# Kernel tuning notes

Measured on AMD Instinct MI355X. Metric: run time of the kernel, lower is better.

## Reference

```python
import jax, jax.numpy as jnp
import numpy as np

N = 100000      # nodes_num
E = 1600000     # edges (avg degree 16)
D_IN = 256
D_OUT = 128
EPS = 1e-3      # keras BatchNormalization default epsilon
LEAKY = 0.2     # tf.nn.leaky_relu default alpha


def setup_inputs() -> dict:
    key = jax.random.key(0)
    ks = jax.random.split(key, 6)
    x = jax.random.normal(ks[0], (N, D_IN), jnp.float32)
    w = jax.random.normal(ks[1], (D_IN, D_OUT), jnp.float32) / np.float32(np.sqrt(D_IN))
    w1 = jax.random.normal(ks[2], (D_IN, D_IN), jnp.float32) / np.float32(np.sqrt(D_IN))
    w2 = jax.random.normal(ks[3], (D_IN, D_IN), jnp.float32) / np.float32(np.sqrt(D_IN))
    rows = jnp.sort(jax.random.randint(ks[4], (E,), 0, N, jnp.int32))
    cols = jax.random.randint(ks[5], (E,), 0, N, jnp.int32)
    edge_vals = jnp.ones((E,), jnp.float32)
    return {"x": x, "w": w, "w1": w1, "w2": w2,
            "edge_vals": edge_vals, "rows": rows, "cols": cols}


def reference(x, w, w1, w2, edge_vals, rows, cols):
    # Batch norm (training mode: per-feature stats over node axis, gamma=1, beta=0)
    mean = jnp.mean(x, axis=0)
    var = jnp.var(x, axis=0)
    xn = (x - mean) * jax.lax.rsqrt(var + EPS)          # [N, D_IN]

    mapped = xn @ w                                      # [N, D_OUT]
    s1 = jnp.tanh(jnp.sum((xn @ w1) * xn, axis=1))       # [N] row score
    s2 = jnp.tanh(jnp.sum((xn @ w2) * xn, axis=1))       # [N] col score

    # sparse add of adj*s1[row] and adj*s2[col], then leaky_relu on edge values
    ev = edge_vals * (s1[rows] + s2[cols])               # [E]
    ev = jnp.where(ev > 0, ev, LEAKY * ev)

    # tf.sparse.softmax: softmax over the nonzero entries of each row
    m = jax.ops.segment_max(ev, rows, num_segments=N)    # [N]
    m = jnp.where(jnp.isfinite(m), m, 0.0)               # empty rows -> 0
    ex = jnp.exp(ev - m[rows])
    denom = jax.ops.segment_sum(ex, rows, num_segments=N)
    alpha = ex / denom[rows]                             # [E] edge softmax

    # SpMM: out[i] = sum_{e: rows[e]==i} alpha[e] * mapped[cols[e]]
    out = jax.ops.segment_sum(alpha[:, None] * mapped[cols], rows, num_segments=N)
    return out  # activation is identity (activation=None)
```

## Files before the change

### kernel.cpp

```cpp
#include <hip/hip_runtime.h>

#define D_IN 256
#define D_OUT 128
#define EPS_BN 1e-3f
#define LEAKY 0.2f

typedef unsigned short u16;
typedef unsigned int u32;
typedef u16 u16x4 __attribute__((ext_vector_type(4)));
typedef u16 u16x8 __attribute__((ext_vector_type(8)));
typedef __bf16 bf16x8 __attribute__((ext_vector_type(8)));
typedef float f32x4 __attribute__((ext_vector_type(4)));

__device__ __forceinline__ float bf2f(u16 u) {
    u32 v = ((u32)u) << 16;
    return __uint_as_float(v);
}
__device__ __forceinline__ u16 f2bf(float f) {
    u32 u = __float_as_uint(f);
    u32 r = (u + 0x7FFFu + ((u >> 16) & 1u)) >> 16;
    return (u16)r;
}

__device__ __forceinline__ void bar_lgkm() {
    asm volatile("s_waitcnt lgkmcnt(0)" ::: "memory");
    __builtin_amdgcn_s_barrier();
    asm volatile("" ::: "memory");
}

__global__ void colstats_k(const float* __restrict__ x, int n,
                           float* __restrict__ sums, float* __restrict__ sqs) {
    int c = threadIdx.x;
    float s = 0.f, q = 0.f;
    for (int r = blockIdx.x; r < n; r += gridDim.x) {
        float v = x[(size_t)r * D_IN + c];
        s += v;
        q += v * v;
    }
    atomicAdd(&sums[c], s);
    atomicAdd(&sqs[c], q);
}

__global__ void finalize_k(const float* __restrict__ sums, const float* __restrict__ sqs,
                           int n, float* __restrict__ mean, float* __restrict__ inv) {
    int c = threadIdx.x;
    float m = sums[c] / (float)n;
    float v = sqs[c] / (float)n - m * m;
    mean[c] = m;
    inv[c] = rsqrtf(v + EPS_BN);
}

__global__ void prep_w_k(const float* __restrict__ w1, const float* __restrict__ w2,
                         const float* __restrict__ w, u16* __restrict__ Bth,
                         u16* __restrict__ Btl, u16* __restrict__ Wth,
                         u16* __restrict__ Wtl) {
    int idx = blockIdx.x * 256 + threadIdx.x;
    int k = idx & 255;
    int nn = idx >> 8;
    if (nn < 512) {
        float v = (nn < 256) ? w1[(size_t)k * 256 + nn]
                             : w2[(size_t)k * 256 + (nn - 256)];
        u16 h = f2bf(v);
        u16 l = f2bf(v - bf2f(h));
        Bth[(size_t)nn * 256 + k] = h;
        Btl[(size_t)nn * 256 + k] = l;
    } else {
        int nm = nn - 512;
        float v = w[(size_t)k * D_OUT + nm];
        u16 h = f2bf(v);
        u16 l = f2bf(v - bf2f(h));
        Wth[(size_t)nm * 256 + k] = h;
        Wtl[(size_t)nm * 256 + k] = l;
    }
}

__device__ __forceinline__ int kmap(int v, int g, int j) {
    return (v == 0) ? (8 * g + j) : (16 * (j >> 2) + 4 * g + (j & 3));
}

__global__ void probe_k(int* __restrict__ flagp) {
    __shared__ float Ar[16][32];
    __shared__ float Br[32][16];
    __shared__ float Dr[16][16];
    int l = threadIdx.x;
    for (int i = l; i < 512; i += 64) {
        int r = i >> 5, k = i & 31;
        Ar[r][k] = (float)(((r * 5 + k * 3) % 11) - 5);
    }
    for (int i = l; i < 512; i += 64) {
        int k = i >> 4, c = i & 15;
        Br[k][c] = (float)(((k * 3 + c * 7) % 13) - 6);
    }
    __syncthreads();
    for (int i = l; i < 256; i += 64) {
        int r = i >> 4, c = i & 15;
        float s = 0.f;
        for (int k = 0; k < 32; ++k) s += Ar[r][k] * Br[k][c];
        Dr[r][c] = s;
    }
    __syncthreads();
    int g = l >> 4, c15 = l & 15;
    int found = -1;
    for (int combo = 0; combo < 4; ++combo) {
        int va = combo >> 1, vb = combo & 1;
        u16x8 af, bfv;
#pragma unroll
        for (int j = 0; j < 8; ++j) {
            af[j] = f2bf(Ar[c15][kmap(va, g, j)]);
            bfv[j] = f2bf(Br[kmap(vb, g, j)][c15]);
        }
        f32x4 d = {0.f, 0.f, 0.f, 0.f};
        d = __builtin_amdgcn_mfma_f32_16x16x32_bf16(
            __builtin_bit_cast(bf16x8, af), __builtin_bit_cast(bf16x8, bfv), d,
            0, 0, 0);
        bool ok = true;
#pragma unroll
        for (int r = 0; r < 4; ++r) ok = ok && (d[r] == Dr[g * 4 + r][c15]);
        if (found < 0 && __all(ok)) found = combo;
    }
    if (l == 0) flagp[0] = (found < 0) ? 0 : found;
}

__device__ __forceinline__ void stage_A(const float* __restrict__ x,
                                        const float* __restrict__ mean,
                                        const float* __restrict__ inv, int m0,
                                        int n, u16* Ah, u16* Al) {
    const int tid = threadIdx.x;
    for (int i = 0; i < 16; ++i) {
        int chunk = tid + (i << 8);
        int r = chunk >> 6;
        int c4 = (chunk & 63) << 2;
        int gr = m0 + r;
        bool ok = gr < n;
        float4 v = make_float4(0.f, 0.f, 0.f, 0.f);
        if (ok) v = *(const float4*)(x + (size_t)gr * D_IN + c4);
        float4 mn = *(const float4*)(mean + c4);
        float4 iv = *(const float4*)(inv + c4);
        float a0 = ok ? (v.x - mn.x) * iv.x : 0.f;
        float a1 = ok ? (v.y - mn.y) * iv.y : 0.f;
        float a2 = ok ? (v.z - mn.z) * iv.z : 0.f;
        float a3 = ok ? (v.w - mn.w) * iv.w : 0.f;
        u16 h0 = f2bf(a0), h1 = f2bf(a1), h2 = f2bf(a2), h3 = f2bf(a3);
        u16 l0 = f2bf(a0 - bf2f(h0)), l1 = f2bf(a1 - bf2f(h1));
        u16 l2 = f2bf(a2 - bf2f(h2)), l3 = f2bf(a3 - bf2f(h3));
        int off = (r << 9) + (((c4 << 1) ^ ((r & 7) << 4)));
        u16x4 hv = {h0, h1, h2, h3};
        u16x4 lv = {l0, l1, l2, l3};
        *(u16x4*)((char*)Ah + off) = hv;
        *(u16x4*)((char*)Al + off) = lv;
    }
}

__device__ __forceinline__ void ldb_regs(const u16* __restrict__ Gh,
                                         const u16* __restrict__ Gl, int n0,
                                         int k0, int tid, u16x8 (&hv)[2],
                                         u16x8 (&lv)[2]) {
#pragma unroll
    for (int i = 0; i < 2; ++i) {
        int chunk = tid + (i << 8);
        int nl = chunk >> 3;
        int k8 = (chunk & 7) << 3;
        size_t goff = (size_t)(n0 + nl) * 256 + k0 + k8;
        hv[i] = *(const u16x8*)(Gh + goff);
        lv[i] = *(const u16x8*)(Gl + goff);
    }
}
__device__ __forceinline__ void stb_lds(u16* Bh, u16* Bl, int tid,
                                        const u16x8 (&hv)[2],
                                        const u16x8 (&lv)[2]) {
#pragma unroll
    for (int i = 0; i < 2; ++i) {
        int chunk = tid + (i << 8);
        int nl = chunk >> 3;
        int k8 = (chunk & 7) << 3;
        int off = (nl << 7) + (((k8 << 1) ^ ((nl & 7) << 4)));
        *(u16x8*)((char*)Bh + off) = hv[i];
        *(u16x8*)((char*)Bl + off) = lv[i];
    }
}

template <int V>
__device__ __forceinline__ bf16x8 ld_frag(const u16* plane, int rowByteBase,
                                          int swz, int kbyte, int g) {
    const char* p = (const char*)plane + rowByteBase;
    if constexpr (V == 0) {
        u16x8 v = *(const u16x8*)(p + ((kbyte + (g << 4)) ^ swz));
        return __builtin_bit_cast(bf16x8, v);
    } else {
        u16x4 a = *(const u16x4*)(p + ((kbyte + (g << 3)) ^ swz));
        u16x4 b = *(const u16x4*)(p + ((kbyte + 32 + (g << 3)) ^ swz));
        u16x8 v;
        v[0] = a[0]; v[1] = a[1]; v[2] = a[2]; v[3] = a[3];
        v[4] = b[0]; v[5] = b[1]; v[6] = b[2]; v[7] = b[3];
        return __builtin_bit_cast(bf16x8, v);
    }
}

template <int VA, int VB>
__device__ __forceinline__ void comp_kt(const u16* Ah, const u16* Al,
                                        const u16* Bh, const u16* Bl, int kt,
                                        int wm, int wn, int c15, int g,
                                        f32x4 (&acc)[2][2]) {
#pragma unroll
    for (int kk = 0; kk < 2; ++kk) {
        int kbA = kt * 128 + kk * 64;
        int kbB = kk * 64;
        bf16x8 ah[2], alf[2], bhf[2], blf[2];
#pragma unroll
        for (int mf = 0; mf < 2; ++mf) {
            int row = wm * 32 + mf * 16 + c15;
            int swz = (row & 7) << 4;
            ah[mf] = ld_frag<VA>(Ah, row << 9, swz, kbA, g);
            alf[mf] = ld_frag<VA>(Al, row << 9, swz, kbA, g);
        }
#pragma unroll
        for (int nf = 0; nf < 2; ++nf) {
            int nl = wn * 32 + nf * 16 + c15;
            int swz = (nl & 7) << 4;
            bhf[nf] = ld_frag<VB>(Bh, nl << 7, swz, kbB, g);
            blf[nf] = ld_frag<VB>(Bl, nl << 7, swz, kbB, g);
        }
#pragma unroll
        for (int mf = 0; mf < 2; ++mf)
#pragma unroll
            for (int nf = 0; nf < 2; ++nf) {
                acc[mf][nf] = __builtin_amdgcn_mfma_f32_16x16x32_bf16(
                    ah[mf], bhf[nf], acc[mf][nf], 0, 0, 0);
                acc[mf][nf] = __builtin_amdgcn_mfma_f32_16x16x32_bf16(
                    ah[mf], blf[nf], acc[mf][nf], 0, 0, 0);
                acc[mf][nf] = __builtin_amdgcn_mfma_f32_16x16x32_bf16(
                    alf[mf], bhf[nf], acc[mf][nf], 0, 0, 0);
            }
    }
}

template <int VA, int VB>
__device__ __forceinline__ void quadmap_body(
    const float* __restrict__ x, const u16* __restrict__ Bth,
    const u16* __restrict__ Btl, const u16* __restrict__ Wth,
    const u16* __restrict__ Wtl, const float* __restrict__ mean,
    const float* __restrict__ inv, float* __restrict__ s1,
    float* __restrict__ s2, u16* __restrict__ mapped, int n, int mapCT,
    u16* Ah, u16* Al, u16* Bh, u16* Bl) {
    const int tid = threadIdx.x;
    const int lane = tid & 63, wave = tid >> 6;
    const int g = lane >> 4, c15 = lane & 15;
    const int wm = wave >> 1, wn = wave & 1;
    const int m0 = blockIdx.x * 64;

    stage_A(x, mean, inv, m0, n, Ah, Al);
    __syncthreads();

    u16x8 rbh[2], rbl[2];
    ldb_regs(Bth, Btl, 0, 0, tid, rbh, rbl);

    float sp[2][4] = {{0.f, 0.f, 0.f, 0.f}, {0.f, 0.f, 0.f, 0.f}};

    for (int jt = 0; jt < 8; ++jt) {
        f32x4 acc[2][2];
#pragma unroll
        for (int mf = 0; mf < 2; ++mf)
#pragma unroll
            for (int nf = 0; nf < 2; ++nf) acc[mf][nf] = (f32x4){0.f, 0.f, 0.f, 0.f};

        for (int kt = 0; kt < 4; ++kt) {
            bar_lgkm();
            stb_lds(Bh, Bl, tid, rbh, rbl);
            const u16 *sH, *sL;
            int nn0, nk0;
            if (kt < 3)      { sH = Bth; sL = Btl; nn0 = jt * 64;       nk0 = (kt + 1) * 64; }
            else if (jt < 7) { sH = Bth; sL = Btl; nn0 = (jt + 1) * 64; nk0 = 0; }
            else             { sH = Wth; sL = Wtl; nn0 = 0;             nk0 = 0; }
            ldb_regs(sH, sL, nn0, nk0, tid, rbh, rbl);
            bar_lgkm();
            comp_kt<VA, VB>(Ah, Al, Bh, Bl, kt, wm, wn, c15, g, acc);
        }

        int fcol0 = (jt & 3) << 6;
#pragma unroll
        for (int mf = 0; mf < 2; ++mf) {
#pragma unroll
            for (int nf = 0; nf < 2; ++nf) {
                int col = fcol0 + wn * 32 + nf * 16 + c15;
                float mn = mean[col], ivv = inv[col];
#pragma unroll
                for (int r = 0; r < 4; ++r) {
                    int grow = m0 + wm * 32 + mf * 16 + g * 4 + r;
                    float xv = 0.f;
                    if (grow < n) xv = (x[(size_t)grow * D_IN + col] - mn) * ivv;
                    sp[mf][r] = fmaf(acc[mf][nf][r], xv, sp[mf][r]);
                }
            }
        }
        if ((jt & 3) == 3) {
            float part[2][4];
#pragma unroll
            for (int mf = 0; mf < 2; ++mf)
#pragma unroll
                for (int r = 0; r < 4; ++r) {
                    float v = sp[mf][r];
                    v += __shfl_xor(v, 1);
                    v += __shfl_xor(v, 2);
                    v += __shfl_xor(v, 4);
                    v += __shfl_xor(v, 8);
                    part[mf][r] = v;
                    sp[mf][r] = 0.f;
                }
            float* scratch = (float*)Bh;
            bar_lgkm();
            if (c15 == 0) {
#pragma unroll
                for (int mf = 0; mf < 2; ++mf)
#pragma unroll
                    for (int r = 0; r < 4; ++r) {
                        int sidx = (((((wm << 2) | g) << 1) | mf) << 3) | (r << 1) | wn;
                        scratch[sidx] = part[mf][r];
                    }
            }
            bar_lgkm();
            if (wn == 0 && c15 == 0) {
                float* dst = (jt < 4) ? s1 : s2;
#pragma unroll
                for (int mf = 0; mf < 2; ++mf)
#pragma unroll
                    for (int r = 0; r < 4; ++r) {
                        int sidx = (((((wm << 2) | g) << 1) | mf) << 3) | (r << 1);
                        float tot = scratch[sidx] + scratch[sidx | 1];
                        int grow = m0 + wm * 32 + mf * 16 + g * 4 + r;
                        if (grow < n) dst[grow] = tanhf(tot);
                    }
            }
        }
    }

    const int tiles = mapCT >> 6;
    for (int t = 0; t < tiles; ++t) {
        f32x4 acc[2][2];
#pragma unroll
        for (int mf = 0; mf < 2; ++mf)
#pragma unroll
            for (int nf = 0; nf < 2; ++nf) acc[mf][nf] = (f32x4){0.f, 0.f, 0.f, 0.f};

        for (int kt = 0; kt < 4; ++kt) {
            bar_lgkm();
            stb_lds(Bh, Bl, tid, rbh, rbl);
            int nn0 = (kt < 3) ? t * 64 : ((t + 1 < tiles) ? (t + 1) * 64 : t * 64);
            int nk0 = (kt < 3) ? (kt + 1) * 64 : 0;
            ldb_regs(Wth, Wtl, nn0, nk0, tid, rbh, rbl);
            bar_lgkm();
            comp_kt<VA, VB>(Ah, Al, Bh, Bl, kt, wm, wn, c15, g, acc);
        }
#pragma unroll
        for (int mf = 0; mf < 2; ++mf)
#pragma unroll
            for (int nf = 0; nf < 2; ++nf) {
                int si = t * 64 + wn * 32 + nf * 16 + c15;
#pragma unroll
                for (int r = 0; r < 4; ++r) {
                    int grow = m0 + wm * 32 + mf * 16 + g * 4 + r;
                    if (grow < n)
                        mapped[(size_t)grow * mapCT + si] = f2bf(acc[mf][nf][r]);
                }
            }
    }
}

__global__ __launch_bounds__(256) void quadmap_mfma_k(
    const float* __restrict__ x, const u16* __restrict__ Bth,
    const u16* __restrict__ Btl, const u16* __restrict__ Wth,
    const u16* __restrict__ Wtl, const float* __restrict__ mean,
    const float* __restrict__ inv, float* __restrict__ s1,
    float* __restrict__ s2, u16* __restrict__ mapped,
    const int* __restrict__ flagp, int n, int mapCT) {
    __shared__ u16 Ah[64 * 256];
    __shared__ u16 Al[64 * 256];
    __shared__ u16 Bh[64 * 64];
    __shared__ u16 Bl[64 * 64];
    int v = flagp[0];
    if (v == 1)
        quadmap_body<0, 1>(x, Bth, Btl, Wth, Wtl, mean, inv, s1, s2, mapped, n, mapCT, Ah, Al, Bh, Bl);
    else if (v == 2)
        quadmap_body<1, 0>(x, Bth, Btl, Wth, Wtl, mean, inv, s1, s2, mapped, n, mapCT, Ah, Al, Bh, Bl);
    else if (v == 3)
        quadmap_body<1, 1>(x, Bth, Btl, Wth, Wtl, mean, inv, s1, s2, mapped, n, mapCT, Ah, Al, Bh, Bl);
    else
        quadmap_body<0, 0>(x, Bth, Btl, Wth, Wtl, mean, inv, s1, s2, mapped, n, mapCT, Ah, Al, Bh, Bl);
}

template <int VA, int VB>
__device__ __forceinline__ void map_body(
    const float* __restrict__ x, const u16* __restrict__ Wth,
    const u16* __restrict__ Wtl, const float* __restrict__ mean,
    const float* __restrict__ inv, u16* __restrict__ mapped, int n, int c0,
    int CT, u16* Ah, u16* Al, u16* Bh, u16* Bl) {
    const int tid = threadIdx.x;
    const int lane = tid & 63, wave = tid >> 6;
    const int g = lane >> 4, c15 = lane & 15;
    const int wm = wave >> 1, wn = wave & 1;
    const int m0 = blockIdx.x * 64;

    stage_A(x, mean, inv, m0, n, Ah, Al);
    __syncthreads();

    u16x8 rbh[2], rbl[2];
    ldb_regs(Wth, Wtl, c0, 0, tid, rbh, rbl);

    const int tiles = CT >> 6;
    for (int t = 0; t < tiles; ++t) {
        f32x4 acc[2][2];
#pragma unroll
        for (int mf = 0; mf < 2; ++mf)
#pragma unroll
            for (int nf = 0; nf < 2; ++nf) acc[mf][nf] = (f32x4){0.f, 0.f, 0.f, 0.f};

        for (int kt = 0; kt < 4; ++kt) {
            bar_lgkm();
            stb_lds(Bh, Bl, tid, rbh, rbl);
            int nn0 = (kt < 3) ? c0 + t * 64
                               : c0 + ((t + 1 < tiles) ? (t + 1) * 64 : t * 64);
            int nk0 = (kt < 3) ? (kt + 1) * 64 : 0;
            ldb_regs(Wth, Wtl, nn0, nk0, tid, rbh, rbl);
            bar_lgkm();
            comp_kt<VA, VB>(Ah, Al, Bh, Bl, kt, wm, wn, c15, g, acc);
        }
#pragma unroll
        for (int mf = 0; mf < 2; ++mf)
#pragma unroll
            for (int nf = 0; nf < 2; ++nf) {
                int si = t * 64 + wn * 32 + nf * 16 + c15;
#pragma unroll
                for (int r = 0; r < 4; ++r) {
                    int grow = m0 + wm * 32 + mf * 16 + g * 4 + r;
                    if (grow < n) mapped[(size_t)grow * CT + si] = f2bf(acc[mf][nf][r]);
                }
            }
    }
}

__global__ __launch_bounds__(256) void map_mfma_k(
    const float* __restrict__ x, const u16* __restrict__ Wth,
    const u16* __restrict__ Wtl, const float* __restrict__ mean,
    const float* __restrict__ inv, u16* __restrict__ mapped, int n, int c0,
    int CT, const int* __restrict__ flagp) {
    __shared__ u16 Ah[64 * 256];
    __shared__ u16 Al[64 * 256];
    __shared__ u16 Bh[64 * 64];
    __shared__ u16 Bl[64 * 64];
    int v = flagp[0];
    if (v == 1) map_body<0, 1>(x, Wth, Wtl, mean, inv, mapped, n, c0, CT, Ah, Al, Bh, Bl);
    else if (v == 2) map_body<1, 0>(x, Wth, Wtl, mean, inv, mapped, n, c0, CT, Ah, Al, Bh, Bl);
    else if (v == 3) map_body<1, 1>(x, Wth, Wtl, mean, inv, mapped, n, c0, CT, Ah, Al, Bh, Bl);
    else map_body<0, 0>(x, Wth, Wtl, mean, inv, mapped, n, c0, CT, Ah, Al, Bh, Bl);
}

template <typename OT>
__global__ __launch_bounds__(256) void gemm_map_k(const float* __restrict__ x,
                                                  const float* __restrict__ w,
                                                  const float* __restrict__ mean,
                                                  const float* __restrict__ inv,
                                                  OT* __restrict__ outp, int n,
                                                  int c0, int CT) {
    __shared__ float As[64][68];
    __shared__ float Bs[64][68];
    const int tid = threadIdx.x;
    const int tx = tid & 15, ty = tid >> 4;
    const int m0 = blockIdx.x * 64;
    const int tiles = (CT + 63) >> 6;

    for (int t = 0; t < tiles; ++t) {
        const int jt = c0 + (t << 6);
        float acc[4][4];
#pragma unroll
        for (int a = 0; a < 4; ++a)
#pragma unroll
            for (int b = 0; b < 4; ++b) acc[a][b] = 0.f;

        for (int kt = 0; kt < D_IN; kt += 64) {
#pragma unroll
            for (int i = 0; i < 4; ++i) {
                int f4 = tid + 256 * i;
                int r = f4 >> 4;
                int c4 = (f4 & 15) << 2;
                float4 o;
                int gr = m0 + r;
                if (gr < n) {
                    float4 v = *(const float4*)(x + (size_t)gr * D_IN + kt + c4);
                    float4 mn = *(const float4*)(mean + kt + c4);
                    float4 iv = *(const float4*)(inv + kt + c4);
                    o.x = (v.x - mn.x) * iv.x;
                    o.y = (v.y - mn.y) * iv.y;
                    o.z = (v.z - mn.z) * iv.z;
                    o.w = (v.w - mn.w) * iv.w;
                } else {
                    o = make_float4(0.f, 0.f, 0.f, 0.f);
                }
                *(float4*)&As[r][c4] = o;
            }
#pragma unroll
            for (int i = 0; i < 4; ++i) {
                int f4 = tid + 256 * i;
                int r = f4 >> 4;
                int c4 = (f4 & 15) << 2;
                int jc = jt + c4;
                float4 bv = (jc < D_OUT)
                                ? *(const float4*)(w + (size_t)(kt + r) * D_OUT + jc)
                                : make_float4(0.f, 0.f, 0.f, 0.f);
                *(float4*)&Bs[r][c4] = bv;
            }
            __syncthreads();
#pragma unroll 8
            for (int k = 0; k < 64; ++k) {
                float4 bv = *(const float4*)&Bs[k][tx << 2];
                float a0 = As[(ty << 2) + 0][k];
                float a1 = As[(ty << 2) + 1][k];
                float a2 = As[(ty << 2) + 2][k];
                float a3 = As[(ty << 2) + 3][k];
                acc[0][0] = fmaf(a0, bv.x, acc[0][0]);
                acc[0][1] = fmaf(a0, bv.y, acc[0][1]);
                acc[0][2] = fmaf(a0, bv.z, acc[0][2]);
                acc[0][3] = fmaf(a0, bv.w, acc[0][3]);
                acc[1][0] = fmaf(a1, bv.x, acc[1][0]);
                acc[1][1] = fmaf(a1, bv.y, acc[1][1]);
                acc[1][2] = fmaf(a1, bv.z, acc[1][2]);
                acc[1][3] = fmaf(a1, bv.w, acc[1][3]);
                acc[2][0] = fmaf(a2, bv.x, acc[2][0]);
                acc[2][1] = fmaf(a2, bv.y, acc[2][1]);
                acc[2][2] = fmaf(a2, bv.z, acc[2][2]);
                acc[2][3] = fmaf(a2, bv.w, acc[2][3]);
                acc[3][0] = fmaf(a3, bv.x, acc[3][0]);
                acc[3][1] = fmaf(a3, bv.y, acc[3][1]);
                acc[3][2] = fmaf(a3, bv.z, acc[3][2]);
                acc[3][3] = fmaf(a3, bv.w, acc[3][3]);
            }
            __syncthreads();
        }
        int si = (jt - c0) + (tx << 2);
        if (si < CT) {
#pragma unroll
            for (int a = 0; a < 4; ++a) {
                int gm = m0 + (ty << 2) + a;
                if (gm < n) {
                    ushort4 pk;
                    pk.x = f2bf(acc[a][0]);
                    pk.y = f2bf(acc[a][1]);
                    pk.z = f2bf(acc[a][2]);
                    pk.w = f2bf(acc[a][3]);
                    *(ushort4*)((u16*)outp + (size_t)gm * CT + si) = pk;
                }
            }
        }
    }
}

__global__ void build_rowptr_k(const int* __restrict__ rows, int E, int n,
                               int* __restrict__ rp) {
    int e = blockIdx.x * blockDim.x + threadIdx.x;
    if (e >= E) return;
    int r = rows[e];
    int prev = (e == 0) ? -1 : rows[e - 1];
    for (int q = prev + 1; q <= r; ++q) rp[q] = e;
    if (e == E - 1) {
        for (int q = r + 1; q <= n; ++q) rp[q] = E;
    }
}

template <bool WRITE_ALPHA>
__global__ __launch_bounds__(256) void row_softmax_k(
    const int* __restrict__ row_ptr, const int* __restrict__ cols,
    const float* __restrict__ ev, const float* __restrict__ s1,
    const float* __restrict__ s2, float* __restrict__ rmax,
    float* __restrict__ rsm, float* __restrict__ alpha, int n) {
    int wave = threadIdx.x >> 6;
    int lane = threadIdx.x & 63;
    int row = blockIdx.x * 4 + wave;
    if (row >= n) return;
    int e0 = row_ptr[row], e1 = row_ptr[row + 1];
    if (e0 >= e1) {
        if (lane == 0) {
            rmax[row] = 0.f;
            rsm[row] = 0.f;
        }
        return;
    }
    float s1r = s1[row];
    float mx = -1e30f;
    for (int e = e0 + lane; e < e1; e += 64) {
        float v = ev[e] * (s1r + s2[cols[e]]);
        v = v > 0.f ? v : LEAKY * v;
        mx = fmaxf(mx, v);
    }
#pragma unroll
    for (int off = 32; off; off >>= 1) mx = fmaxf(mx, __shfl_xor(mx, off));
    float sm = 0.f;
    for (int e = e0 + lane; e < e1; e += 64) {
        float v = ev[e] * (s1r + s2[cols[e]]);
        v = v > 0.f ? v : LEAKY * v;
        sm += __expf(v - mx);
    }
#pragma unroll
    for (int off = 32; off; off >>= 1) sm += __shfl_xor(sm, off);
    float rsm_v = 1.f / sm;
    if (lane == 0) {
        rmax[row] = mx;
        rsm[row] = rsm_v;
    }
    if constexpr (WRITE_ALPHA) {
        for (int e = e0 + lane; e < e1; e += 64) {
            float v = ev[e] * (s1r + s2[cols[e]]);
            v = v > 0.f ? v : LEAKY * v;
            alpha[e] = __expf(v - mx) * rsm_v;
        }
    }
}

template <bool HAS_ALPHA>
__global__ __launch_bounds__(256) void attn_gather2_k(
    const int* __restrict__ row_ptr, const int* __restrict__ cols,
    const float* __restrict__ alpha, const float* __restrict__ ev,
    const float* __restrict__ s1, const float* __restrict__ s2,
    const float* __restrict__ rmax, const float* __restrict__ rsm,
    const u16* __restrict__ mapped, float* __restrict__ outp, int n, int c0,
    int CT) {
    const int wave = threadIdx.x >> 6;
    const int lane = threadIdx.x & 63;
    const int row = blockIdx.x * 4 + wave;
    if (row >= n) return;
    const int e0 = row_ptr[row], e1 = row_ptr[row + 1];
    float* orow = outp + (size_t)row * D_OUT + c0;
    const int nu = CT >> 1;
    const bool act = lane < nu;
    if (e0 >= e1) {
        if (act) *(float2*)(orow + (lane << 1)) = make_float2(0.f, 0.f);
        return;
    }
    float s1r = 0.f, mxv = 0.f, rsv = 0.f;
    if constexpr (!HAS_ALPHA) {
        s1r = s1[row];
        mxv = rmax[row];
        rsv = rsm[row];
    }
    const u32* map32 = (const u32*)mapped;
    float ox = 0.f, oy = 0.f;
    int e = e0;
    while (e < e1) {
        int cnt = min(e1 - e, 64);
        int ce = 0;
        float ae = 0.f;
        if (lane < cnt) {
            int ee = e + lane;
            ce = cols[ee];
            if constexpr (HAS_ALPHA) {
                ae = alpha[ee];
            } else {
                float v = ev[ee] * (s1r + s2[ce]);
                v = v > 0.f ? v : LEAKY * v;
                ae = __expf(v - mxv) * rsv;
            }
        }
        for (int j0 = 0; j0 < cnt; j0 += 8) {
            int cv[8];
            float av[8];
            u32 mv[8];
#pragma unroll
            for (int j = 0; j < 8; ++j) {
                cv[j] = __shfl(ce, j0 + j);
                av[j] = __shfl(ae, j0 + j);
            }
#pragma unroll
            for (int j = 0; j < 8; ++j)
                mv[j] = act ? map32[(size_t)cv[j] * nu + lane] : 0u;
#pragma unroll
            for (int j = 0; j < 8; ++j) {
                ox = fmaf(av[j], bf2f((u16)(mv[j] & 0xffffu)), ox);
                oy = fmaf(av[j], bf2f((u16)(mv[j] >> 16)), oy);
            }
        }
        e += cnt;
    }
    if (act) *(float2*)(orow + (lane << 1)) = make_float2(ox, oy);
}

extern "C" void kernel_launch(void* const* d_in, const int* in_sizes, int n_in,
                              void* d_out, int out_size, void* d_ws, size_t ws_size,
                              hipStream_t stream) {
    const float* x  = (const float*)d_in[0];
    const float* w  = (const float*)d_in[1];
    const float* w1 = (const float*)d_in[2];
    const float* w2 = (const float*)d_in[3];
    const float* ev = (const float*)d_in[4];
    const int* rows = (const int*)d_in[5];
    const int* cols = (const int*)d_in[6];
    float* out = (float*)d_out;

    const int N = in_sizes[0] / D_IN;
    const int E = in_sizes[4];

    char* base = (char*)d_ws;
    size_t off = 0;
    auto alloc = [&](size_t bytes) -> char* {
        off = (off + 255) & ~(size_t)255;
        char* p = base + off;
        off += bytes;
        return p;
    };
    float* sums  = (float*)alloc(256 * 4);
    float* sqs   = (float*)alloc(256 * 4);
    float* mean  = (float*)alloc(256 * 4);
    float* inv   = (float*)alloc(256 * 4);
    float* s1    = (float*)alloc((size_t)N * 4);
    float* s2    = (float*)alloc((size_t)N * 4);
    float* rmax  = (float*)alloc((size_t)N * 4);
    float* rsm   = (float*)alloc((size_t)N * 4);
    int* row_ptr = (int*)alloc((size_t)(N + 1) * 4);
    int* flag    = (int*)alloc(256);
    u16* Bth = (u16*)alloc((size_t)512 * 256 * 2);
    u16* Btl = (u16*)alloc((size_t)512 * 256 * 2);
    u16* Wth = (u16*)alloc((size_t)128 * 256 * 2);
    u16* Wtl = (u16*)alloc((size_t)128 * 256 * 2);
    size_t head0 = off;

    size_t alpha_bytes = (size_t)E * 4;
    auto fits_alpha = [&](size_t mapped_bytes) {
        size_t o = (head0 + 255) & ~(size_t)255;
        o += alpha_bytes;
        o = (o + 255) & ~(size_t)255;
        return o + mapped_bytes <= ws_size;
    };
    auto fits_noalpha = [&](size_t mapped_bytes) {
        size_t o = (head0 + 255) & ~(size_t)255;
        return o + mapped_bytes <= ws_size;
    };

    bool has_alpha;
    int CT;
    if (fits_alpha((size_t)N * 128 * 2)) {
        has_alpha = true; CT = 128;
    } else if (fits_alpha((size_t)N * 64 * 2)) {
        has_alpha = true; CT = 64;
    } else if (fits_noalpha((size_t)N * 32 * 2)) {
        has_alpha = false; CT = 32;
    } else if (fits_noalpha((size_t)N * 16 * 2)) {
        has_alpha = false; CT = 16;
    } else {
        has_alpha = false; CT = 8;
    }
    float* alpha = has_alpha ? (float*)alloc(alpha_bytes) : nullptr;
    u16* mapped = (u16*)alloc((size_t)N * CT * 2);

    hipMemsetAsync(sums, 0, 512 * sizeof(float), stream);
    colstats_k<<<512, 256, 0, stream>>>(x, N, sums, sqs);
    finalize_k<<<1, 256, 0, stream>>>(sums, sqs, N, mean, inv);
    prep_w_k<<<640, 256, 0, stream>>>(w1, w2, w, Bth, Btl, Wth, Wtl);
    probe_k<<<1, 64, 0, stream>>>(flag);

    int qb = (N + 63) / 64;
    int mapCT = (CT >= 64) ? CT : 0;
    quadmap_mfma_k<<<qb, 256, 0, stream>>>(x, Bth, Btl, Wth, Wtl, mean, inv, s1,
                                           s2, mapped, flag, N, mapCT);

    build_rowptr_k<<<(E + 255) / 256, 256, 0, stream>>>(rows, E, N, row_ptr);
    int ab = (N + 3) / 4;
    if (has_alpha) {
        row_softmax_k<true><<<ab, 256, 0, stream>>>(row_ptr, cols, ev, s1, s2,
                                                    rmax, rsm, alpha, N);
    } else {
        row_softmax_k<false><<<ab, 256, 0, stream>>>(row_ptr, cols, ev, s1, s2,
                                                     rmax, rsm, nullptr, N);
    }

    if (CT == 128) {
        attn_gather2_k<true><<<ab, 256, 0, stream>>>(
            row_ptr, cols, alpha, ev, s1, s2, rmax, rsm, mapped, out, N, 0, CT);
    } else if (CT == 64) {
        attn_gather2_k<true><<<ab, 256, 0, stream>>>(
            row_ptr, cols, alpha, ev, s1, s2, rmax, rsm, mapped, out, N, 0, 64);
        map_mfma_k<<<qb, 256, 0, stream>>>(x, Wth, Wtl, mean, inv, mapped, N, 64,
                                           64, flag);
        attn_gather2_k<true><<<ab, 256, 0, stream>>>(
            row_ptr, cols, alpha, ev, s1, s2, rmax, rsm, mapped, out, N, 64, 64);
    } else {
        for (int c0 = 0; c0 < D_OUT; c0 += CT) {
            gemm_map_k<u16><<<qb, 256, 0, stream>>>(x, w, mean, inv, mapped, N,
                                                    c0, CT);
            attn_gather2_k<false><<<ab, 256, 0, stream>>>(
                row_ptr, cols, nullptr, ev, s1, s2, rmax, rsm, mapped, out, N,
                c0, CT);
        }
    }
}
```

Baseline: 584.7 us.

## Retile quadmap GEMM to 64x128 output tiles with 32-wide K stages

The fused quadratic-score/mapping MFMA kernel now computes 64x128 output tiles per block, each wave covering 32x64 with 8 accumulators, and streams B in 128x32 K-slices instead of 64x64. This halves the number of passes over the staged A tile and gives each B fragment more MFMA reuse. The cost is more accumulator registers and a barrier every 32 K. Mapping inside this kernel is limited to the full CT=128 case, and the CT=64 path now launches a separate map kernel for the first half.

Result: no change. 581.2 us (-0.6%).

```diff
diff --git a/kernel.cpp b/kernel.cpp
--- a/kernel.cpp
+++ b/kernel.cpp
@@ -121,13 +121,15 @@
     if (l == 0) flagp[0] = (found < 0) ? 0 : found;
 }
 
+template <int NT>
 __device__ __forceinline__ void stage_A(const float* __restrict__ x,
                                         const float* __restrict__ mean,
                                         const float* __restrict__ inv, int m0,
                                         int n, u16* Ah, u16* Al) {
     const int tid = threadIdx.x;
-    for (int i = 0; i < 16; ++i) {
-        int chunk = tid + (i << 8);
+#pragma unroll
+    for (int i = 0; i < 4096 / NT; ++i) {
+        int chunk = tid + i * NT;
         int r = chunk >> 6;
         int c4 = (chunk & 63) << 2;
         int gr = m0 + r;
@@ -151,34 +153,6 @@
     }
 }
 
-__device__ __forceinline__ void ldb_regs(const u16* __restrict__ Gh,
-                                         const u16* __restrict__ Gl, int n0,
-                                         int k0, int tid, u16x8 (&hv)[2],
-                                         u16x8 (&lv)[2]) {
-#pragma unroll
-    for (int i = 0; i < 2; ++i) {
-        int chunk = tid + (i << 8);
-        int nl = chunk >> 3;
-        int k8 = (chunk & 7) << 3;
-        size_t goff = (size_t)(n0 + nl) * 256 + k0 + k8;
-        hv[i] = *(const u16x8*)(Gh + goff);
-        lv[i] = *(const u16x8*)(Gl + goff);
-    }
-}
-__device__ __forceinline__ void stb_lds(u16* Bh, u16* Bl, int tid,
-                                        const u16x8 (&hv)[2],
-                                        const u16x8 (&lv)[2]) {
-#pragma unroll
-    for (int i = 0; i < 2; ++i) {
-        int chunk = tid + (i << 8);
-        int nl = chunk >> 3;
-        int k8 = (chunk & 7) << 3;
-        int off = (nl << 7) + (((k8 << 1) ^ ((nl & 7) << 4)));
-        *(u16x8*)((char*)Bh + off) = hv[i];
-        *(u16x8*)((char*)Bl + off) = lv[i];
-    }
-}
-
 template <int V>
 __device__ __forceinline__ bf16x8 ld_frag(const u16* plane, int rowByteBase,
                                           int swz, int kbyte, int g) {
@@ -196,41 +170,97 @@
     }
 }
 
+__device__ __forceinline__ void ldb2(const u16* __restrict__ Gh,
+                                     const u16* __restrict__ Gl, int n0, int k0,
+                                     int tid, u16x8 (&hv)[2], u16x8 (&lv)[2]) {
+#pragma unroll
+    for (int i = 0; i < 2; ++i) {
+        int chunk = tid + (i << 8);
+        int nl = chunk >> 2;
+        int k8 = (chunk & 3) << 3;
+        size_t goff = (size_t)(n0 + nl) * 256 + k0 + k8;
+        hv[i] = *(const u16x8*)(Gh + goff);
+        lv[i] = *(const u16x8*)(Gl + goff);
+    }
+}
+__device__ __forceinline__ void stb2(u16* Bh, u16* Bl, int tid,
+                                     const u16x8 (&hv)[2], const u16x8 (&lv)[2]) {
+#pragma unroll
+    for (int i = 0; i < 2; ++i) {
+        int chunk = tid + (i << 8);
+        int nl = chunk >> 2;
+        int kb = (chunk & 3) << 4;
+        int off = (nl << 6) + (kb ^ (((nl >> 1) & 3) << 4));
+        *(u16x8*)((char*)Bh + off) = hv[i];
+        *(u16x8*)((char*)Bl + off) = lv[i];
+    }
+}
+template <int V>
+__device__ __forceinline__ bf16x8 ld_bfrag(const u16* Bp, int nl, int g) {
+    const char* p = (const char*)Bp + (nl << 6);
+    int swz = ((nl >> 1) & 3) << 4;
+    if constexpr (V == 0) {
+        u16x8 v = *(const u16x8*)(p + ((g << 4) ^ swz));
+        return __builtin_bit_cast(bf16x8, v);
+    } else {
+        u16x4 a = *(const u16x4*)(p + ((g << 3) ^ swz));
+        u16x4 b = *(const u16x4*)(p + ((32 + (g << 3)) ^ swz));
+        u16x8 v;
+        v[0] = a[0]; v[1] = a[1]; v[2] = a[2]; v[3] = a[3];
+        v[4] = b[0]; v[5] = b[1]; v[6] = b[2]; v[7] = b[3];
+        return __builtin_bit_cast(bf16x8, v);
+    }
+}
+
 template <int VA, int VB>
-__device__ __forceinline__ void comp_kt(const u16* Ah, const u16* Al,
-                                        const u16* Bh, const u16* Bl, int kt,
-                                        int wm, int wn, int c15, int g,
-                                        f32x4 (&acc)[2][2]) {
-#pragma unroll
-    for (int kk = 0; kk < 2; ++kk) {
-        int kbA = kt * 128 + kk * 64;
-        int kbB = kk * 64;
-        bf16x8 ah[2], alf[2], bhf[2], blf[2];
-#pragma unroll
-        for (int mf = 0; mf < 2; ++mf) {
-            int row = wm * 32 + mf * 16 + c15;
-            int swz = (row & 7) << 4;
-            ah[mf] = ld_frag<VA>(Ah, row << 9, swz, kbA, g);
-            alf[mf] = ld_frag<VA>(Al, row << 9, swz, kbA, g);
-        }
-#pragma unroll
-        for (int nf = 0; nf < 2; ++nf) {
-            int nl = wn * 32 + nf * 16 + c15;
-            int swz = (nl & 7) << 4;
-            bhf[nf] = ld_frag<VB>(Bh, nl << 7, swz, kbB, g);
-            blf[nf] = ld_frag<VB>(Bl, nl << 7, swz, kbB, g);
-        }
-#pragma unroll
-        for (int mf = 0; mf < 2; ++mf)
-#pragma unroll
-            for (int nf = 0; nf < 2; ++nf) {
-                acc[mf][nf] = __builtin_amdgcn_mfma_f32_16x16x32_bf16(
-                    ah[mf], bhf[nf], acc[mf][nf], 0, 0, 0);
-                acc[mf][nf] = __builtin_amdgcn_mfma_f32_16x16x32_bf16(
-                    ah[mf], blf[nf], acc[mf][nf], 0, 0, 0);
-                acc[mf][nf] = __builtin_amdgcn_mfma_f32_16x16x32_bf16(
-                    alf[mf], bhf[nf], acc[mf][nf], 0, 0, 0);
-            }
+__device__ __forceinline__ void comp32(const u16* Ah, const u16* Al,
+                                       const u16* Bh, const u16* Bl, int kbA,
+                                       int wm, int wj, int c15, int g,
+                                       f32x4 (&acc)[2][4]) {
+    bf16x8 ah[2], alf[2];
+#pragma unroll
+    for (int mf = 0; mf < 2; ++mf) {
+        int row = wm * 32 + mf * 16 + c15;
+        int swz = (row & 7) << 4;
+        ah[mf] = ld_frag<VA>(Ah, row << 9, swz, kbA, g);
+        alf[mf] = ld_frag<VA>(Al, row << 9, swz, kbA, g);
+    }
+    bf16x8 bh[4], bl[4];
+#pragma unroll
+    for (int nf = 0; nf < 4; ++nf) {
+        int nl = wj * 64 + nf * 16 + c15;
+        bh[nf] = ld_bfrag<VB>(Bh, nl, g);
+        bl[nf] = ld_bfrag<VB>(Bl, nl, g);
+    }
+#pragma unroll
+    for (int mf = 0; mf < 2; ++mf)
+#pragma unroll
+        for (int nf = 0; nf < 4; ++nf) {
+            acc[mf][nf] = __builtin_amdgcn_mfma_f32_16x16x32_bf16(
+                ah[mf], bh[nf], acc[mf][nf], 0, 0, 0);
+            acc[mf][nf] = __builtin_amdgcn_mfma_f32_16x16x32_bf16(
+                ah[mf], bl[nf], acc[mf][nf], 0, 0, 0);
+            acc[mf][nf] = __builtin_amdgcn_mfma_f32_16x16x32_bf16(
+                alf[mf], bh[nf], acc[mf][nf], 0, 0, 0);
+        }
+}
+
+__device__ __forceinline__ void nxt_src2(int u, int totSub,
+                                         const u16* __restrict__ Bth,
+                                         const u16* __restrict__ Btl,
+                                         const u16* __restrict__ Wth,
+                                         const u16* __restrict__ Wtl,
+                                         const u16*& Gh, const u16*& Gl,
+                                         int& n0, int& k0) {
+    if (u >= totSub) u = totSub - 1;
+    if (u < 32) {
+        Gh = Bth; Gl = Btl;
+        n0 = (u >> 3) << 7;
+        k0 = (u & 7) << 5;
+    } else {
+        Gh = Wth; Gl = Wtl;
+        n0 = 0;
+        k0 = (u & 7) << 5;
     }
 }
 
@@ -245,54 +275,61 @@
     const int tid = threadIdx.x;
     const int lane = tid & 63, wave = tid >> 6;
     const int g = lane >> 4, c15 = lane & 15;
-    const int wm = wave >> 1, wn = wave & 1;
+    const int wm = wave >> 1, wj = wave & 1;
     const int m0 = blockIdx.x * 64;
 
-    stage_A(x, mean, inv, m0, n, Ah, Al);
+    stage_A<256>(x, mean, inv, m0, n, Ah, Al);
     __syncthreads();
 
-    u16x8 rbh[2], rbl[2];
-    ldb_regs(Bth, Btl, 0, 0, tid, rbh, rbl);
+    const int totSub = 32 + ((mapCT == 128) ? 8 : 0);
+    u16x8 rh[2], rl[2];
+    {
+        const u16 *Gh, *Gl; int n0, k0;
+        nxt_src2(0, totSub, Bth, Btl, Wth, Wtl, Gh, Gl, n0, k0);
+        ldb2(Gh, Gl, n0, k0, tid, rh, rl);
+    }
 
     float sp[2][4] = {{0.f, 0.f, 0.f, 0.f}, {0.f, 0.f, 0.f, 0.f}};
-
-    for (int jt = 0; jt < 8; ++jt) {
-        f32x4 acc[2][2];
+    float* red = (float*)Bh;
+
+    for (int p = 0; p < 4; ++p) {
+        f32x4 acc[2][4];
 #pragma unroll
         for (int mf = 0; mf < 2; ++mf)
 #pragma unroll
-            for (int nf = 0; nf < 2; ++nf) acc[mf][nf] = (f32x4){0.f, 0.f, 0.f, 0.f};
-
-        for (int kt = 0; kt < 4; ++kt) {
+            for (int nf = 0; nf < 4; ++nf) acc[mf][nf] = (f32x4){0.f, 0.f, 0.f, 0.f};
+
+#pragma unroll
+        for (int u8 = 0; u8 < 8; ++u8) {
             bar_lgkm();
-            stb_lds(Bh, Bl, tid, rbh, rbl);
-            const u16 *sH, *sL;
-            int nn0, nk0;
-            if (kt < 3)      { sH = Bth; sL = Btl; nn0 = jt * 64;       nk0 = (kt + 1) * 64; }
-            else if (jt < 7) { sH = Bth; sL = Btl; nn0 = (jt + 1) * 64; nk0 = 0; }
-            else             { sH = Wth; sL = Wtl; nn0 = 0;             nk0 = 0; }
-            ldb_regs(sH, sL, nn0, nk0, tid, rbh, rbl);
+            stb2(Bh, Bl, tid, rh, rl);
+            const u16 *Gh, *Gl; int n0, k0;
+            nxt_src2(p * 8 + u8 + 1, totSub, Bth, Btl, Wth, Wtl, Gh, Gl, n0, k0);
+            ldb2(Gh, Gl, n0, k0, tid, rh, rl);
             bar_lgkm();
-            comp_kt<VA, VB>(Ah, Al, Bh, Bl, kt, wm, wn, c15, g, acc);
-        }
-
-        int fcol0 = (jt & 3) << 6;
-#pragma unroll
-        for (int mf = 0; mf < 2; ++mf) {
-#pragma unroll
-            for (int nf = 0; nf < 2; ++nf) {
-                int col = fcol0 + wn * 32 + nf * 16 + c15;
+            comp32<VA, VB>(Ah, Al, Bh, Bl, u8 * 64, wm, wj, c15, g, acc);
+        }
+
+        {
+            int jtg = p * 2 + wj;
+            int fcol0 = (jtg & 3) << 6;
+#pragma unroll
+            for (int nf = 0; nf < 4; ++nf) {
+                int col = fcol0 + nf * 16 + c15;
                 float mn = mean[col], ivv = inv[col];
 #pragma unroll
-                for (int r = 0; r < 4; ++r) {
-                    int grow = m0 + wm * 32 + mf * 16 + g * 4 + r;
-                    float xv = 0.f;
-                    if (grow < n) xv = (x[(size_t)grow * D_IN + col] - mn) * ivv;
-                    sp[mf][r] = fmaf(acc[mf][nf][r], xv, sp[mf][r]);
+                for (int mf = 0; mf < 2; ++mf) {
+#pragma unroll
+                    for (int r = 0; r < 4; ++r) {
+                        int grow = m0 + wm * 32 + mf * 16 + g * 4 + r;
+                        float xv = 0.f;
+                        if (grow < n) xv = (x[(size_t)grow * D_IN + col] - mn) * ivv;
+                        sp[mf][r] = fmaf(acc[mf][nf][r], xv, sp[mf][r]);
+                    }
                 }
             }
         }
-        if ((jt & 3) == 3) {
+        if (p & 1) {
             float part[2][4];
 #pragma unroll
             for (int mf = 0; mf < 2; ++mf)
@@ -306,26 +343,25 @@
                     part[mf][r] = v;
                     sp[mf][r] = 0.f;
                 }
-            float* scratch = (float*)Bh;
             bar_lgkm();
             if (c15 == 0) {
 #pragma unroll
                 for (int mf = 0; mf < 2; ++mf)
 #pragma unroll
                     for (int r = 0; r < 4; ++r) {
-                        int sidx = (((((wm << 2) | g) << 1) | mf) << 3) | (r << 1) | wn;
-                        scratch[sidx] = part[mf][r];
+                        int sidx = (((((wm << 2) | g) << 1) | mf) << 3) | (r << 1) | wj;
+                        red[sidx] = part[mf][r];
                     }
             }
             bar_lgkm();
-            if (wn == 0 && c15 == 0) {
-                float* dst = (jt < 4) ? s1 : s2;
+            if (wj == 0 && c15 == 0) {
+                float* dst = (p < 2) ? s1 : s2;
 #pragma unroll
                 for (int mf = 0; mf < 2; ++mf)
 #pragma unroll
                     for (int r = 0; r < 4; ++r) {
                         int sidx = (((((wm << 2) | g) << 1) | mf) << 3) | (r << 1);
-                        float tot = scratch[sidx] + scratch[sidx | 1];
+                        float tot = red[sidx] + red[sidx | 1];
                         int grow = m0 + wm * 32 + mf * 16 + g * 4 + r;
                         if (grow < n) dst[grow] = tanhf(tot);
                     }
@@ -333,33 +369,33 @@
         }
     }
 
-    const int tiles = mapCT >> 6;
-    for (int t = 0; t < tiles; ++t) {
-        f32x4 acc[2][2];
+    if (mapCT == 128) {
+        f32x4 acc[2][4];
 #pragma unroll
         for (int mf = 0; mf < 2; ++mf)
 #pragma unroll
-            for (int nf = 0; nf < 2; ++nf) acc[mf][nf] = (f32x4){0.f, 0.f, 0.f, 0.f};
-
-        for (int kt = 0; kt < 4; ++kt) {
+            for (int nf = 0; nf < 4; ++nf) acc[mf][nf] = (f32x4){0.f, 0.f, 0.f, 0.f};
+
+#pragma unroll
+        for (int u8 = 0; u8 < 8; ++u8) {
             bar_lgkm();
-            stb_lds(Bh, Bl, tid, rbh, rbl);
-            int nn0 = (kt < 3) ? t * 64 : ((t + 1 < tiles) ? (t + 1) * 64 : t * 64);
-            int nk0 = (kt < 3) ? (kt + 1) * 64 : 0;
-            ldb_regs(Wth, Wtl, nn0, nk0, tid, rbh, rbl);
+            stb2(Bh, Bl, tid, rh, rl);
+            const u16 *Gh, *Gl; int n0, k0;
+            nxt_src2(32 + u8 + 1, totSub, Bth, Btl, Wth, Wtl, Gh, Gl, n0, k0);
+            ldb2(Gh, Gl, n0, k0, tid, rh, rl);
             bar_lgkm();
-            comp_kt<VA, VB>(Ah, Al, Bh, Bl, kt, wm, wn, c15, g, acc);
+            comp32<VA, VB>(Ah, Al, Bh, Bl, u8 * 64, wm, wj, c15, g, acc);
         }
 #pragma unroll
         for (int mf = 0; mf < 2; ++mf)
 #pragma unroll
-            for (int nf = 0; nf < 2; ++nf) {
-                int si = t * 64 + wn * 32 + nf * 16 + c15;
+            for (int nf = 0; nf < 4; ++nf) {
+                int si = wj * 64 + nf * 16 + c15;
 #pragma unroll
                 for (int r = 0; r < 4; ++r) {
                     int grow = m0 + wm * 32 + mf * 16 + g * 4 + r;
                     if (grow < n)
-                        mapped[(size_t)grow * mapCT + si] = f2bf(acc[mf][nf][r]);
+                        mapped[(size_t)grow * 128 + si] = f2bf(acc[mf][nf][r]);
                 }
             }
     }
@@ -374,8 +410,8 @@
     const int* __restrict__ flagp, int n, int mapCT) {
     __shared__ u16 Ah[64 * 256];
     __shared__ u16 Al[64 * 256];
-    __shared__ u16 Bh[64 * 64];
-    __shared__ u16 Bl[64 * 64];
+    __shared__ u16 Bh[128 * 32];
+    __shared__ u16 Bl[128 * 32];
     int v = flagp[0];
     if (v == 1)
         quadmap_body<0, 1>(x, Bth, Btl, Wth, Wtl, mean, inv, s1, s2, mapped, n, mapCT, Ah, Al, Bh, Bl);
@@ -385,6 +421,71 @@
         quadmap_body<1, 1>(x, Bth, Btl, Wth, Wtl, mean, inv, s1, s2, mapped, n, mapCT, Ah, Al, Bh, Bl);
     else
         quadmap_body<0, 0>(x, Bth, Btl, Wth, Wtl, mean, inv, s1, s2, mapped, n, mapCT, Ah, Al, Bh, Bl);
+}
+
+__device__ __forceinline__ void ldb_regs(const u16* __restrict__ Gh,
+                                         const u16* __restrict__ Gl, int n0,
+                                         int k0, int tid, u16x8 (&hv)[2],
+                                         u16x8 (&lv)[2]) {
+#pragma unroll
+    for (int i = 0; i < 2; ++i) {
+        int chunk = tid + (i << 8);
+        int nl = chunk >> 3;
+        int k8 = (chunk & 7) << 3;
+        size_t goff = (size_t)(n0 + nl) * 256 + k0 + k8;
+        hv[i] = *(const u16x8*)(Gh + goff);
+        lv[i] = *(const u16x8*)(Gl + goff);
+    }
+}
+__device__ __forceinline__ void stb_lds(u16* Bh, u16* Bl, int tid,
+                                        const u16x8 (&hv)[2],
+                                        const u16x8 (&lv)[2]) {
+#pragma unroll
+    for (int i = 0; i < 2; ++i) {
+        int chunk = tid + (i << 8);
+        int nl = chunk >> 3;
+        int k8 = (chunk & 7) << 3;
+        int off = (nl << 7) + (((k8 << 1) ^ ((nl & 7) << 4)));
+        *(u16x8*)((char*)Bh + off) = hv[i];
+        *(u16x8*)((char*)Bl + off) = lv[i];
+    }
+}
+template <int VA, int VB>
+__device__ __forceinline__ void comp_kt(const u16* Ah, const u16* Al,
+                                        const u16* Bh, const u16* Bl, int kt,
+                                        int wm, int wn, int c15, int g,
+                                        f32x4 (&acc)[2][2]) {
+#pragma unroll
+    for (int kk = 0; kk < 2; ++kk) {
+        int kbA = kt * 128 + kk * 64;
+        int kbB = kk * 64;
+        bf16x8 ah[2], alf[2], bhf[2], blf[2];
+#pragma unroll
+        for (int mf = 0; mf < 2; ++mf) {
+            int row = wm * 32 + mf * 16 + c15;
+            int swz = (row & 7) << 4;
+            ah[mf] = ld_frag<VA>(Ah, row << 9, swz, kbA, g);
+            alf[mf] = ld_frag<VA>(Al, row << 9, swz, kbA, g);
+        }
+#pragma unroll
+        for (int nf = 0; nf < 2; ++nf) {
+            int nl = wn * 32 + nf * 16 + c15;
+            int swz = (nl & 7) << 4;
+            bhf[nf] = ld_frag<VB>(Bh, nl << 7, swz, kbB, g);
+            blf[nf] = ld_frag<VB>(Bl, nl << 7, swz, kbB, g);
+        }
+#pragma unroll
+        for (int mf = 0; mf < 2; ++mf)
+#pragma unroll
+            for (int nf = 0; nf < 2; ++nf) {
+                acc[mf][nf] = __builtin_amdgcn_mfma_f32_16x16x32_bf16(
+                    ah[mf], bhf[nf], acc[mf][nf], 0, 0, 0);
+                acc[mf][nf] = __builtin_amdgcn_mfma_f32_16x16x32_bf16(
+                    ah[mf], blf[nf], acc[mf][nf], 0, 0, 0);
+                acc[mf][nf] = __builtin_amdgcn_mfma_f32_16x16x32_bf16(
+                    alf[mf], bhf[nf], acc[mf][nf], 0, 0, 0);
+            }
+    }
 }
 
 template <int VA, int VB>
@@ -399,7 +500,7 @@
     const int wm = wave >> 1, wn = wave & 1;
     const int m0 = blockIdx.x * 64;
 
-    stage_A(x, mean, inv, m0, n, Ah, Al);
+    stage_A<256>(x, mean, inv, m0, n, Ah, Al);
     __syncthreads();
 
     u16x8 rbh[2], rbl[2];
@@ -754,7 +855,7 @@
     probe_k<<<1, 64, 0, stream>>>(flag);
 
     int qb = (N + 63) / 64;
-    int mapCT = (CT >= 64) ? CT : 0;
+    int mapCT = (CT == 128) ? 128 : 0;
     quadmap_mfma_k<<<qb, 256, 0, stream>>>(x, Bth, Btl, Wth, Wtl, mean, inv, s1,
                                            s2, mapped, flag, N, mapCT);
 
@@ -772,6 +873,8 @@
         attn_gather2_k<true><<<ab, 256, 0, stream>>>(
             row_ptr, cols, alpha, ev, s1, s2, rmax, rsm, mapped, out, N, 0, CT);
     } else if (CT == 64) {
+        map_mfma_k<<<qb, 256, 0, stream>>>(x, Wth, Wtl, mean, inv, mapped, N, 0,
+                                           64, flag);
         attn_gather2_k<true><<<ab, 256, 0, stream>>>(
             row_ptr, cols, alpha, ev, s1, s2, rmax, rsm, mapped, out, N, 0, 64);
         map_mfma_k<<<qb, 256, 0, stream>>>(x, Wth, Wtl, mean, inv, mapped, N, 64,
```
